# Kernel tuning notes

Hardware: AMD Instinct MI355X
Metric: run time of the kernel (lower is better)

## Reference

```python
import jax, jax.numpy as jnp
import numpy as np

V, D, S, L, H, R, W = 32000, 512, 1536, 4, 4, 32, 128
HFF = int(2.0 * D)
N = S + 1          # anchor node at index 0 + S tokens
K = W + 2          # anchor edge + (W+1) causal window edges
LN_EPS = 1e-5


def _layer_norm(x, g, b):
    m = jnp.mean(x, axis=-1, keepdims=True)
    v = jnp.mean((x - m) ** 2, axis=-1, keepdims=True)
    return (x - m) * jax.lax.rsqrt(v + LN_EPS) * g + b


def _neighbors():
    # windowed causal neighborhood: node i sees nodes i-W..i, plus anchor (node 0)
    pos = jnp.arange(N)
    offs = jnp.arange(-W, 1)                     # W+1 offsets
    idx_w = pos[:, None] + offs[None, :]         # [N, W+1]
    valid_w = idx_w >= 0
    idx_w = jnp.maximum(idx_w, 0)
    anchor_valid = (pos > W)[:, None]            # avoid double-counting anchor when already in window
    idx = jnp.concatenate([jnp.zeros((N, 1), idx_w.dtype), idx_w], axis=1)   # [N, K]
    mask = jnp.concatenate([anchor_valid, valid_w], axis=1)                  # [N, K]
    return idx, mask


def setup_inputs() -> dict:
    key = jax.random.key(0)
    ks = jax.random.split(key, 10)
    std = 0.02
    return {
        'input_ids': jax.random.randint(ks[0], (1, S), 0, V),
        'embed': jax.random.normal(ks[1], (V, D), jnp.float32) * std,
        'pos_emb': jax.random.normal(ks[2], (S, D), jnp.float32) * std,
        'ln_in_g': jnp.ones((D,), jnp.float32),
        'ln_in_b': jnp.zeros((D,), jnp.float32),
        'anchor_state': jnp.zeros((), jnp.float32),
        'anchor_val': jax.random.normal(ks[3], (D,), jnp.float32) * std,
        'state_w': jax.random.normal(ks[4], (D,), jnp.float32) * std,
        'state_b': jnp.zeros((), jnp.float32),
        'wq': jax.random.normal(ks[5], (L, H, D, R), jnp.float32) * std,
        'wk': jax.random.normal(ks[6], (L, H, D, R), jnp.float32) * std,
        'gate': jnp.full((L,), 0.1, jnp.float32),
        'ln_g': jnp.ones((L, D), jnp.float32),
        'ln_b': jnp.zeros((L, D), jnp.float32),
        'ffn_w1': jax.random.normal(ks[7], (L, D, HFF), jnp.float32) * std,
        'ffn_b1': jnp.zeros((L, HFF), jnp.float32),
        'ffn_w2': jax.random.normal(ks[8], (L, HFF, D), jnp.float32) * std,
        'ffn_b2': jnp.zeros((L, D), jnp.float32),
        'ln2_g': jnp.ones((L, D), jnp.float32),
        'ln2_b': jnp.zeros((L, D), jnp.float32),
    }


def reference(input_ids, embed, pos_emb, ln_in_g, ln_in_b, anchor_state, anchor_val,
              state_w, state_b, wq, wk, gate, ln_g, ln_b,
              ffn_w1, ffn_b1, ffn_w2, ffn_b2, ln2_g, ln2_b):
    B = input_ids.shape[0]
    # token embedding + learned position encoding + input norm
    tok = embed[input_ids] + pos_emb[None]                 # [B,S,D]
    tok = _layer_norm(tok, ln_in_g, ln_in_b)
    tok_state = tok @ state_w + state_b                    # [B,S] scalar state per node
    # prepend anchor node
    val = jnp.concatenate([jnp.broadcast_to(anchor_val, (B, 1, D)), tok], axis=1)       # [B,N,D]
    state = jnp.concatenate([jnp.broadcast_to(anchor_state, (B, 1)), tok_state], axis=1)  # [B,N]
    idx, mask = _neighbors()
    scale = 1.0 / np.sqrt(R)
    for l in range(L):
        # low-rank multi-head pairwise scores on windowed neighborhood
        q = jnp.einsum('bnd,hdr->bnhr', val, wq[l])
        k = jnp.einsum('bnd,hdr->bnhr', val, wk[l])
        kg = k[:, idx]                                     # [B,N,K,H,R] gather
        s = jnp.einsum('bnhr,bnkhr->bnkh', q, kg) * scale  # [B,N,K,H]
        # signed_smoothmax head aggregation
        hw = jax.nn.softmax(jnp.abs(s), axis=-1)
        a = jnp.sum(s * hw, axis=-1)                       # [B,N,K]
        # signed_abs_softmax edge compression over neighborhood
        absa = jnp.where(mask[None], jnp.abs(a), -jnp.inf)
        e = jnp.sign(a) * jax.nn.softmax(absa, axis=-1)    # masked entries -> 0 weight
        # state-weighted edges
        sg = state[:, idx]                                 # [B,N,K]
        e = e * sg
        val_g = val[:, idx]                                # [B,N,K,D]
        d_val = jnp.einsum('bnk,bnkd->bnd', e, val_g)
        d_state = jnp.sum(e, axis=-1)
        # gated residual + post-norm
        state = state + gate[l] * d_state
        val = val + gate[l] * d_val
        val = _layer_norm(val, ln_g[l], ln_b[l])
        # value feed-forward (pre-norm, residual scale 1.0)
        h = jax.nn.gelu(_layer_norm(val, ln2_g[l], ln2_b[l]) @ ffn_w1[l] + ffn_b1[l], approximate=False)
        val = val + h @ ffn_w2[l] + ffn_b2[l]
    return val
```

## Files before the change

kernel.cpp:

```cpp
#include <hip/hip_runtime.h>
#include <hip/hip_bf16.h>
#include <stdint.h>

namespace {

constexpr int D    = 512;
constexpr int S    = 1536;
constexpr int N    = S + 1;
constexpr int L    = 4;
constexpr int H    = 4;
constexpr int R    = 32;
constexpr int W    = 128;
constexpr int HFF  = 1024;
constexpr float EPS = 1e-5f;

constexpr int TB   = 4;
constexpr int NB4  = (N + TB - 1) / TB;
constexpr int SP   = 133;
constexpr int SPAD = 137;

constexpr int GS2  = 1024;
constexpr int SLABR = 528;
constexpr int BK   = 128;

typedef __attribute__((ext_vector_type(8))) short short8;
typedef __attribute__((ext_vector_type(4))) float floatx4;

__device__ inline ushort f2bf(float x){
  __hip_bfloat16 h = __float2bfloat16(x);
  return *reinterpret_cast<ushort*>(&h);
}
__device__ inline float bf2f(uint u){
  union { uint u; float f; } c; c.u = u << 16; return c.f;
}

__device__ inline float wave_sum(float v){
#pragma unroll
  for (int o = 32; o; o >>= 1) v += __shfl_xor(v, o, 64);
  return v;
}
__device__ inline float wave_max(float v){
#pragma unroll
  for (int o = 32; o; o >>= 1) v = fmaxf(v, __shfl_xor(v, o, 64));
  return v;
}
__device__ inline float block_sum(float v, float* scr){
  v = wave_sum(v);
  __syncthreads();
  if ((threadIdx.x & 63) == 0) scr[threadIdx.x >> 6] = v;
  __syncthreads();
  return scr[0] + scr[1] + scr[2] + scr[3];
}

__global__ __launch_bounds__(256) void setup_kernel(
    const int* __restrict__ ids, const float* __restrict__ embed,
    const float* __restrict__ pos, const float* __restrict__ g,
    const float* __restrict__ b, const float* __restrict__ anchor_val,
    const float* __restrict__ anchor_state, const float* __restrict__ state_w,
    const float* __restrict__ state_b, float* __restrict__ val,
    ushort* __restrict__ valbf, float* __restrict__ state,
    const float* __restrict__ wq, const float* __restrict__ wk,
    ushort* __restrict__ wqkbf,
    const float* __restrict__ ffn_w1, const float* __restrict__ ffn_w2,
    ushort* __restrict__ w1t, ushort* __restrict__ w2t)
{
  __shared__ float scr[4];
  __shared__ float tile[32 * 33];
  const int t = threadIdx.x;

  for (int n = blockIdx.x; n < N; n += GS2){
    if (n == 0){
      float a0 = anchor_val[t], a1 = anchor_val[t + 256];
      val[t] = a0; val[t + 256] = a1;
      valbf[t] = f2bf(a0); valbf[t + 256] = f2bf(a1);
      if (t == 0) state[0] = anchor_state[0];
      continue;
    }
    int tp = n - 1;
    int id = ids[tp];
    float x0 = embed[(size_t)id * D + t]       + pos[tp * D + t];
    float x1 = embed[(size_t)id * D + t + 256] + pos[tp * D + t + 256];
    float mean = block_sum(x0 + x1, scr) * (1.f / D);
    float var  = block_sum(x0 * x0 + x1 * x1, scr) * (1.f / D) - mean * mean;
    float rs   = rsqrtf(var + EPS);
    float y0 = (x0 - mean) * rs * g[t]       + b[t];
    float y1 = (x1 - mean) * rs * g[t + 256] + b[t + 256];
    val[n * D + t]       = y0;
    val[n * D + t + 256] = y1;
    valbf[n * D + t]       = f2bf(y0);
    valbf[n * D + t + 256] = f2bf(y1);
    float ts = block_sum(y0 * state_w[t] + y1 * state_w[t + 256], scr);
    if (t == 0) state[n] = ts + state_b[0];
  }

  for (int i = blockIdx.x * 256 + t; i < L * 256 * D; i += GS2 * 256){
    int d = i & 511;
    int c = (i >> 9) & 255;
    int l = i >> 17;
    int cc = c & 127;
    int h = cc >> 5, r = cc & 31;
    const float* src = (c < 128) ? wq : wk;
    wqkbf[i] = f2bf(src[((l * H + h) * D + d) * R + r]);
  }
  __syncthreads();

  const int tx = t & 31, ty = t >> 5;
  for (int tl = blockIdx.x; tl < 2 * L * 512; tl += GS2){
    const float* s; ushort* dd; int rows, cols, c0, r0;
    if (tl < 2048){
      int ll = tl >> 9, i = tl & 511;
      rows = D; cols = HFF;
      s  = ffn_w1 + (size_t)ll * D * HFF;
      dd = w1t   + (size_t)ll * D * HFF;
      c0 = (i & 31) << 5; r0 = (i >> 5) << 5;
    } else {
      int tl2 = tl - 2048;
      int ll = tl2 >> 9, i = tl2 & 511;
      rows = HFF; cols = D;
      s  = ffn_w2 + (size_t)ll * D * HFF;
      dd = w2t   + (size_t)ll * D * HFF;
      c0 = (i & 15) << 5; r0 = (i >> 4) << 5;
    }
    __syncthreads();
    for (int rr = ty; rr < 32; rr += 8)
      tile[rr * 33 + tx] = s[(size_t)(r0 + rr) * cols + c0 + tx];
    __syncthreads();
    for (int rr = ty; rr < 32; rr += 8)
      dd[(size_t)(c0 + rr) * rows + r0 + tx] = f2bf(tile[tx * 33 + rr]);
  }
}

template<int ACT>
__global__ __launch_bounds__(256) void gemm64(
    const ushort* __restrict__ A, const ushort* __restrict__ Bt,
    const float* __restrict__ bias, const float* __restrict__ resid,
    float* __restrict__ C, ushort* __restrict__ Cbf,
    int M, int Kd, int Nc)
{
  __shared__ ushort As[16 * SLABR];
  __shared__ ushort Bs[16 * SLABR];
  const int row0 = blockIdx.y * 64;
  const int col0 = blockIdx.x * 64;
  const int t = threadIdx.x;
  const int lane = t & 63, w = t >> 6;
  const int wr = w & 1, wc = w >> 1;
  const int q = lane >> 4, lm = lane & 15;

  const int srow = t >> 3, skb = t & 7;
  int ar0 = min(row0 + srow,      M - 1);
  int ar1 = min(row0 + srow + 32, M - 1);
  const ushort* agA0 = A  + (size_t)ar0 * Kd + skb * 8;
  const ushort* agA1 = A  + (size_t)ar1 * Kd + skb * 8;
  const ushort* agB0 = Bt + (size_t)(col0 + srow) * Kd + skb * 8;
  const ushort* agB1 = Bt + (size_t)(col0 + srow + 32) * Kd + skb * 8;
  ushort* asw00 = &As[ skb      * SLABR +  srow       * 8];
  ushort* asw01 = &As[(skb + 8) * SLABR +  srow       * 8];
  ushort* asw10 = &As[ skb      * SLABR + (srow + 32) * 8];
  ushort* asw11 = &As[(skb + 8) * SLABR + (srow + 32) * 8];
  ushort* bsw00 = &Bs[ skb      * SLABR +  srow       * 8];
  ushort* bsw01 = &Bs[(skb + 8) * SLABR +  srow       * 8];
  ushort* bsw10 = &Bs[ skb      * SLABR + (srow + 32) * 8];
  ushort* bsw11 = &Bs[(skb + 8) * SLABR + (srow + 32) * 8];

  const ushort* arp = &As[(wr * 32 + lm) * 8];
  const ushort* brp = &Bs[(wc * 32 + lm) * 8];

  floatx4 acc[2][2];
#pragma unroll
  for (int m = 0; m < 2; ++m)
#pragma unroll
    for (int n = 0; n < 2; ++n) acc[m][n] = {0.f, 0.f, 0.f, 0.f};

  const int nk0 = Kd / BK;
  uint4 pa0, pa1, pa2, pa3, pb0, pb1, pb2, pb3;
  pa0 = *(const uint4*)(agA0);      pa1 = *(const uint4*)(agA0 + 64);
  pa2 = *(const uint4*)(agA1);      pa3 = *(const uint4*)(agA1 + 64);
  pb0 = *(const uint4*)(agB0);      pb1 = *(const uint4*)(agB0 + 64);
  pb2 = *(const uint4*)(agB1);      pb3 = *(const uint4*)(agB1 + 64);

  for (int i = 0; i < nk0; ++i){
    *(uint4*)asw00 = pa0; *(uint4*)asw01 = pa1;
    *(uint4*)asw10 = pa2; *(uint4*)asw11 = pa3;
    *(uint4*)bsw00 = pb0; *(uint4*)bsw01 = pb1;
    *(uint4*)bsw10 = pb2; *(uint4*)bsw11 = pb3;
    __syncthreads();
    if (i + 1 < nk0){
      const int ko = (i + 1) * BK;
      pa0 = *(const uint4*)(agA0 + ko);      pa1 = *(const uint4*)(agA0 + ko + 64);
      pa2 = *(const uint4*)(agA1 + ko);      pa3 = *(const uint4*)(agA1 + ko + 64);
      pb0 = *(const uint4*)(agB0 + ko);      pb1 = *(const uint4*)(agB0 + ko + 64);
      pb2 = *(const uint4*)(agB1 + ko);      pb3 = *(const uint4*)(agB1 + ko + 64);
    }
#pragma unroll
    for (int kk = 0; kk < 4; ++kk){
      const int kb = (kk * 4 + q) * SLABR;
      short8 am0 = *(const short8*)(arp + kb);
      short8 am1 = *(const short8*)(arp + kb + 16 * 8);
      short8 bn0 = *(const short8*)(brp + kb);
      short8 bn1 = *(const short8*)(brp + kb + 16 * 8);
      acc[0][0] = __builtin_amdgcn_mfma_f32_16x16x32_bf16(am0, bn0, acc[0][0], 0, 0, 0);
      acc[0][1] = __builtin_amdgcn_mfma_f32_16x16x32_bf16(am0, bn1, acc[0][1], 0, 0, 0);
      acc[1][0] = __builtin_amdgcn_mfma_f32_16x16x32_bf16(am1, bn0, acc[1][0], 0, 0, 0);
      acc[1][1] = __builtin_amdgcn_mfma_f32_16x16x32_bf16(am1, bn1, acc[1][1], 0, 0, 0);
    }
    __syncthreads();
  }

#pragma unroll
  for (int m = 0; m < 2; ++m){
#pragma unroll
    for (int n = 0; n < 2; ++n){
      int col = col0 + wc * 32 + n * 16 + lm;
#pragma unroll
      for (int r = 0; r < 4; ++r){
        int row = row0 + wr * 32 + m * 16 + q * 4 + r;
        if (row >= M) continue;
        float v = acc[m][n][r] + (bias ? bias[col] : 0.f);
        if (ACT == 1) v = 0.5f * v * (1.f + erff(v * 0.70710678118654752f));
        if (resid) v += resid[(size_t)row * Nc + col];
        size_t o = (size_t)row * Nc + col;
        if (C)   C[o] = v;
        if (Cbf) Cbf[o] = f2bf(v);
      }
    }
  }
}

__global__ __launch_bounds__(256) void attn4_kernel(
    const ushort* __restrict__ qkbf, const float* __restrict__ val0,
    const ushort* __restrict__ val0bf, const float* __restrict__ state_in,
    float* __restrict__ val1, ushort* __restrict__ x2bf,
    float* __restrict__ state_out,
    const float* __restrict__ gate_p, const float* __restrict__ lng,
    const float* __restrict__ lnb, const float* __restrict__ ln2g,
    const float* __restrict__ ln2b)
{
  __shared__ float kg[64 * SPAD];
  __shared__ float qsh[TB * 128];
  __shared__ float ssh[16 * SPAD];
  __shared__ float ash[TB * SPAD];
  const int n0 = blockIdx.x * TB;
  const int t = threadIdx.x;
  const int w = t >> 6, l = t & 63;
  const float gate = gate_p[0];
  const float scale = 0.17677669529663687f;

#pragma unroll
  for (int i = t; i < TB * 128; i += 256){
    int it = i >> 7, ch = i & 127;
    int gr = min(n0 + it, N - 1);
    qsh[i] = bf2f((uint)qkbf[(size_t)gr * 256 + ch]);
  }

  for (int half = 0; half < 2; ++half){
    for (int i = t; i < SP * 16; i += 256){
      int c = i >> 4, c4 = i & 15;
      int g = (c == 132) ? 0 : min(max(n0 - W + c, 0), N - 1);
      uint2 v = *(const uint2*)&qkbf[(size_t)g * 256 + 128 + half * 64 + c4 * 4];
      int ch = c4 * 4;
      kg[(ch + 0) * SPAD + c] = bf2f(v.x & 0xffffu);
      kg[(ch + 1) * SPAD + c] = bf2f(v.x >> 16);
      kg[(ch + 2) * SPAD + c] = bf2f(v.y & 0xffffu);
      kg[(ch + 3) * SPAD + c] = bf2f(v.y >> 16);
    }
    __syncthreads();
    for (int tk = t; tk < TB * 2 * SP; tk += 256){
      int c = tk % SP;
      int th = tk / SP;
      int tok = th & 3, hh = th >> 2;
      int h = half * 2 + hh;
      const float* qs = &qsh[tok * 128 + h * 32];
      const float* ks = &kg[hh * 32 * SPAD + c];
      float acc = 0.f;
#pragma unroll
      for (int r = 0; r < 32; ++r) acc += qs[r] * ks[r * SPAD];
      ssh[(tok * 4 + h) * SPAD + c] = acc * scale;
    }
    __syncthreads();
  }

  for (int i = t; i < TB * SP; i += 256){
    int tok = i / SP, c = i - tok * SP;
    const float* sr = &ssh[tok * 4 * SPAD + c];
    float s0 = sr[0], s1 = sr[SPAD], s2 = sr[2 * SPAD], s3 = sr[3 * SPAD];
    float a0 = fabsf(s0), a1 = fabsf(s1), a2 = fabsf(s2), a3 = fabsf(s3);
    float m = fmaxf(fmaxf(a0, a1), fmaxf(a2, a3));
    float w0 = expf(a0 - m), w1 = expf(a1 - m), w2 = expf(a2 - m), w3 = expf(a3 - m);
    ash[tok * SPAD + c] = (s0 * w0 + s1 * w1 + s2 * w2 + s3 * w3) / (w0 + w1 + w2 + w3);
  }
  __syncthreads();

  {
    const int n = n0 + w;
    float* arow = &ash[w * SPAD];
    float a0 = arow[l];
    float a1 = arow[64 + l];
    float a2 = (l < 5) ? arow[128 + l] : 0.f;
    bool ok0 = (l >= w) && (n0 - W + l >= 0);
    bool ok1 = (n0 - W + 64 + l >= 0);
    bool ok2;
    if (l < 4)       ok2 = (l <= w);
    else if (l == 4) ok2 = (n > W);
    else             ok2 = false;
    float cand = -3.4e38f;
    if (ok0) cand = fabsf(a0);
    if (ok1) cand = fmaxf(cand, fabsf(a1));
    if (ok2) cand = fmaxf(cand, fabsf(a2));
    float m = wave_max(cand);
    float e0 = ok0 ? expf(fabsf(a0) - m) : 0.f;
    float e1 = ok1 ? expf(fabsf(a1) - m) : 0.f;
    float e2 = ok2 ? expf(fabsf(a2) - m) : 0.f;
    float inv = 1.f / wave_sum(e0 + e1 + e2);
    int g0 = min(max(n0 - W + l, 0), N - 1);
    int g1 = min(max(n0 - W + 64 + l, 0), N - 1);
    int g2 = (l < 4) ? min(n0 + l, N - 1) : 0;
    float sg0 = (a0 > 0.f) ? 1.f : ((a0 < 0.f) ? -1.f : 0.f);
    float sg1 = (a1 > 0.f) ? 1.f : ((a1 < 0.f) ? -1.f : 0.f);
    float sg2 = (a2 > 0.f) ? 1.f : ((a2 < 0.f) ? -1.f : 0.f);
    float t0 = sg0 * e0 * inv * state_in[g0];
    float t1 = sg1 * e1 * inv * state_in[g1];
    float t2 = (l < 5) ? sg2 * e2 * inv * state_in[g2] : 0.f;
    arow[l] = t0;
    arow[64 + l] = t1;
    if (l < 5) arow[128 + l] = t2;
    float ds = wave_sum(t0 + t1 + t2);
    if (l == 0 && n < N) state_out[n] = state_in[n] + gate * ds;
  }
  __syncthreads();

  float acc[TB][2];
#pragma unroll
  for (int k = 0; k < TB; ++k){ acc[k][0] = 0.f; acc[k][1] = 0.f; }
  {
    const int d0 = 2 * t;
    for (int c = 0; c < SP; ++c){
      int g = (c == 132) ? 0 : min(max(n0 - W + c, 0), N - 1);
      uint v = *(const uint*)&val0bf[(size_t)g * D + d0];
      float vx = bf2f(v & 0xffffu), vy = bf2f(v >> 16);
#pragma unroll
      for (int k = 0; k < TB; ++k){
        float e = ash[k * SPAD + c];
        acc[k][0] += e * vx;
        acc[k][1] += e * vy;
      }
    }
  }
  float* xbuf = kg;
  {
    const int d0 = 2 * t;
#pragma unroll
    for (int k = 0; k < TB; ++k){
      int nc = min(n0 + k, N - 1);
      float2 vv = *(const float2*)&val0[(size_t)nc * D + d0];
      xbuf[k * 520 + d0]     = vv.x + gate * acc[k][0];
      xbuf[k * 520 + d0 + 1] = vv.y + gate * acc[k][1];
    }
  }
  __syncthreads();

  {
    const int n = n0 + w;
    const int d = l * 8;
    const float* xr = &xbuf[w * 520 + d];
    float x[8];
#pragma unroll
    for (int j = 0; j < 8; ++j) x[j] = xr[j];
    float s1 = 0.f, s2 = 0.f;
#pragma unroll
    for (int j = 0; j < 8; ++j){ s1 += x[j]; s2 += x[j] * x[j]; }
    s1 = wave_sum(s1); s2 = wave_sum(s2);
    float mean = s1 * (1.f / D);
    float var  = s2 * (1.f / D) - mean * mean;
    float rs   = rsqrtf(var + EPS);
    float y[8];
    float u1 = 0.f, u2 = 0.f;
#pragma unroll
    for (int j = 0; j < 8; ++j){
      float yv = (x[j] - mean) * rs * lng[d + j] + lnb[d + j];
      y[j] = yv; u1 += yv; u2 += yv * yv;
    }
    u1 = wave_sum(u1); u2 = wave_sum(u2);
    float mean2 = u1 * (1.f / D);
    float var2  = u2 * (1.f / D) - mean2 * mean2;
    float rs2   = rsqrtf(var2 + EPS);
    if (n < N){
      *(float4*)&val1[(size_t)n * D + d]     = make_float4(y[0], y[1], y[2], y[3]);
      *(float4*)&val1[(size_t)n * D + d + 4] = make_float4(y[4], y[5], y[6], y[7]);
      uint4 pk;
      uint z0 = f2bf((y[0] - mean2) * rs2 * ln2g[d + 0] + ln2b[d + 0]);
      uint z1 = f2bf((y[1] - mean2) * rs2 * ln2g[d + 1] + ln2b[d + 1]);
      uint z2 = f2bf((y[2] - mean2) * rs2 * ln2g[d + 2] + ln2b[d + 2]);
      uint z3 = f2bf((y[3] - mean2) * rs2 * ln2g[d + 3] + ln2b[d + 3]);
      uint z4 = f2bf((y[4] - mean2) * rs2 * ln2g[d + 4] + ln2b[d + 4]);
      uint z5 = f2bf((y[5] - mean2) * rs2 * ln2g[d + 5] + ln2b[d + 5]);
      uint z6 = f2bf((y[6] - mean2) * rs2 * ln2g[d + 6] + ln2b[d + 6]);
      uint z7 = f2bf((y[7] - mean2) * rs2 * ln2g[d + 7] + ln2b[d + 7]);
      pk.x = z0 | (z1 << 16); pk.y = z2 | (z3 << 16);
      pk.z = z4 | (z5 << 16); pk.w = z6 | (z7 << 16);
      *(uint4*)&x2bf[(size_t)n * D + d] = pk;
    }
  }
}

}

extern "C" void kernel_launch(void* const* d_in, const int* in_sizes, int n_in,
                              void* d_out, int out_size, void* d_ws, size_t ws_size,
                              hipStream_t stream)
{
  (void)in_sizes; (void)n_in; (void)out_size; (void)ws_size;
  const int*   ids          = (const int*)d_in[0];
  const float* embed        = (const float*)d_in[1];
  const float* pos_emb      = (const float*)d_in[2];
  const float* ln_in_g      = (const float*)d_in[3];
  const float* ln_in_b      = (const float*)d_in[4];
  const float* anchor_state = (const float*)d_in[5];
  const float* anchor_val   = (const float*)d_in[6];
  const float* state_w      = (const float*)d_in[7];
  const float* state_b      = (const float*)d_in[8];
  const float* wq           = (const float*)d_in[9];
  const float* wk           = (const float*)d_in[10];
  const float* gate         = (const float*)d_in[11];
  const float* ln_g         = (const float*)d_in[12];
  const float* ln_b         = (const float*)d_in[13];
  const float* ffn_w1       = (const float*)d_in[14];
  const float* ffn_b1       = (const float*)d_in[15];
  const float* ffn_w2       = (const float*)d_in[16];
  const float* ffn_b2       = (const float*)d_in[17];
  const float* ln2_g        = (const float*)d_in[18];
  const float* ln2_b        = (const float*)d_in[19];
  float* out = (float*)d_out;

  float* wsf  = (float*)d_ws;
  float* val0 = wsf;  wsf += (size_t)N * D;
  float* val1 = wsf;  wsf += (size_t)N * D;
  ushort* wsu   = (ushort*)wsf;
  ushort* val0bf = wsu;  wsu += (size_t)N * D;
  ushort* x2bf   = wsu;  wsu += (size_t)N * D;
  ushort* hbf    = wsu;  wsu += (size_t)N * HFF;
  ushort* qkbf   = wsu;  wsu += (size_t)N * 256;
  ushort* wqkbf  = wsu;  wsu += (size_t)L * 256 * D;
  ushort* w1t    = wsu;  wsu += (size_t)L * HFF * D;
  ushort* w2t    = wsu;  wsu += (size_t)L * HFF * D;
  float* st0 = (float*)wsu;
  float* st1 = st0 + N;

  setup_kernel<<<GS2, 256, 0, stream>>>(
      ids, embed, pos_emb, ln_in_g, ln_in_b, anchor_val, anchor_state,
      state_w, state_b, val0, val0bf, st0,
      wq, wk, wqkbf, ffn_w1, ffn_w2, w1t, w2t);

  float* sin_  = st0;
  float* sout_ = st1;
  const int MT64 = (N + 63) / 64;
  for (int l = 0; l < L; ++l){
    gemm64<0><<<dim3(256 / 64, MT64), 256, 0, stream>>>(
        val0bf, wqkbf + (size_t)l * 256 * D, nullptr, nullptr,
        nullptr, qkbf, N, D, 256);
    attn4_kernel<<<NB4, 256, 0, stream>>>(qkbf, val0, val0bf, sin_, val1, x2bf,
                                          sout_, gate + l, ln_g + l * D,
                                          ln_b + l * D, ln2_g + l * D,
                                          ln2_b + l * D);
    gemm64<1><<<dim3(HFF / 64, MT64), 256, 0, stream>>>(
        x2bf, w1t + (size_t)l * HFF * D, ffn_b1 + l * HFF, nullptr,
        nullptr, hbf, N, D, HFF);
    float* dst = (l == L - 1) ? out : val0;
    gemm64<0><<<dim3(D / 64, MT64), 256, 0, stream>>>(
        hbf, w2t + (size_t)l * HFF * D, ffn_b2 + l * D, val1,
        dst, val0bf, N, HFF, D);
    float* tmp = sin_; sin_ = sout_; sout_ = tmp;
  }
}
```

Before: 374.9 us.

## Fuse Q/K projection into attention kernel, recomputing window keys per block

Removes the separate Q/K projection GEMM and its bf16 round trip through global memory. Each attention block now computes its own 4 query rows and the keys for its 133-row window with bf16 MFMA, staging val0bf and the projection weights in shared memory. This saves one launch and the intermediate buffer. In exchange, each block recomputes keys for a window that overlaps heavily with its neighbours, so total projection work grows many-fold. Each block also re-reads the full projection weight slice.

```diff
diff --git a/kernel.cpp b/kernel.cpp
--- a/kernel.cpp
+++ b/kernel.cpp
@@ -22,6 +22,10 @@
 constexpr int GS2  = 1024;
 constexpr int SLABR = 528;
 constexpr int BK   = 128;
+
+constexpr int KROWS = 144;
+constexpr int SLABK = KROWS * 8 + 8;
+constexpr int BSLAB = 64 * 8 + 8;
 
 typedef __attribute__((ext_vector_type(8))) short short8;
 typedef __attribute__((ext_vector_type(4))) float floatx4;
@@ -226,8 +230,9 @@
   }
 }
 
-__global__ __launch_bounds__(256) void attn4_kernel(
-    const ushort* __restrict__ qkbf, const float* __restrict__ val0,
+__global__ __launch_bounds__(256) void qkattn_kernel(
+    const ushort* __restrict__ wqk,
+    const float* __restrict__ val0,
     const ushort* __restrict__ val0bf, const float* __restrict__ state_in,
     float* __restrict__ val1, ushort* __restrict__ x2bf,
     float* __restrict__ state_out,
@@ -239,29 +244,99 @@
   __shared__ float qsh[TB * 128];
   __shared__ float ssh[16 * SPAD];
   __shared__ float ash[TB * SPAD];
+  __shared__ ushort As2[8 * SLABK];
+  __shared__ ushort Bs2[8 * BSLAB];
   const int n0 = blockIdx.x * TB;
   const int t = threadIdx.x;
   const int w = t >> 6, l = t & 63;
+  const int q = l >> 4, lm = l & 15;
   const float gate = gate_p[0];
   const float scale = 0.17677669529663687f;
 
-#pragma unroll
-  for (int i = t; i < TB * 128; i += 256){
-    int it = i >> 7, ch = i & 127;
-    int gr = min(n0 + it, N - 1);
-    qsh[i] = bf2f((uint)qkbf[(size_t)gr * 256 + ch]);
-  }
+  {
+    floatx4 accq0 = {0.f,0.f,0.f,0.f}, accq1 = {0.f,0.f,0.f,0.f};
+    for (int ks = 0; ks < 8; ++ks){
+      if (t < 128){
+        int row = t >> 3, kb = t & 7;
+        int g = min(n0 + row, N - 1);
+        *(uint4*)&Bs2[kb * BSLAB + row * 8] =
+            *(const uint4*)&val0bf[(size_t)g * D + ks * 64 + kb * 8];
+      }
+#pragma unroll
+      for (int s = 0; s < 4; ++s){
+        int slot = t + s * 256;
+        int ch = slot >> 3, kb = slot & 7;
+        *(uint4*)&As2[kb * SLABK + ch * 8] =
+            *(const uint4*)&wqk[(size_t)ch * D + ks * 64 + kb * 8];
+      }
+      __syncthreads();
+#pragma unroll
+      for (int kk = 0; kk < 2; ++kk){
+        int kc = kk * 4 + q;
+        short8 a  = *(const short8*)&Bs2[kc * BSLAB + lm * 8];
+        short8 b0 = *(const short8*)&As2[kc * SLABK + ((2 * w)     * 16 + lm) * 8];
+        short8 b1 = *(const short8*)&As2[kc * SLABK + ((2 * w + 1) * 16 + lm) * 8];
+        accq0 = __builtin_amdgcn_mfma_f32_16x16x32_bf16(a, b0, accq0, 0, 0, 0);
+        accq1 = __builtin_amdgcn_mfma_f32_16x16x32_bf16(a, b1, accq1, 0, 0, 0);
+      }
+      __syncthreads();
+    }
+    if (q == 0){
+#pragma unroll
+      for (int r = 0; r < 4; ++r){
+        qsh[r * 128 + (2 * w)     * 16 + lm] = accq0[r];
+        qsh[r * 128 + (2 * w + 1) * 16 + lm] = accq1[r];
+      }
+    }
+  }
+  __syncthreads();
 
   for (int half = 0; half < 2; ++half){
-    for (int i = t; i < SP * 16; i += 256){
-      int c = i >> 4, c4 = i & 15;
-      int g = (c == 132) ? 0 : min(max(n0 - W + c, 0), N - 1);
-      uint2 v = *(const uint2*)&qkbf[(size_t)g * 256 + 128 + half * 64 + c4 * 4];
-      int ch = c4 * 4;
-      kg[(ch + 0) * SPAD + c] = bf2f(v.x & 0xffffu);
-      kg[(ch + 1) * SPAD + c] = bf2f(v.x >> 16);
-      kg[(ch + 2) * SPAD + c] = bf2f(v.y & 0xffffu);
-      kg[(ch + 3) * SPAD + c] = bf2f(v.y >> 16);
+    floatx4 acck[9];
+#pragma unroll
+    for (int tr = 0; tr < 9; ++tr) acck[tr] = {0.f, 0.f, 0.f, 0.f};
+    for (int ks = 0; ks < 8; ++ks){
+#pragma unroll
+      for (int s = 0; s < 5; ++s){
+        int slot = t + s * 256;
+        if (slot < KROWS * 8){
+          int row = slot >> 3, kb = slot & 7;
+          int g = (row == 132) ? 0 : min(max(n0 - W + row, 0), N - 1);
+          *(uint4*)&As2[kb * SLABK + row * 8] =
+              *(const uint4*)&val0bf[(size_t)g * D + ks * 64 + kb * 8];
+        }
+      }
+#pragma unroll
+      for (int s = 0; s < 2; ++s){
+        int slot = t + s * 256;
+        int ch = slot >> 3, kb = slot & 7;
+        *(uint4*)&Bs2[kb * BSLAB + ch * 8] =
+            *(const uint4*)&wqk[(size_t)(128 + half * 64 + ch) * D + ks * 64 + kb * 8];
+      }
+      __syncthreads();
+#pragma unroll
+      for (int kk = 0; kk < 2; ++kk){
+        int kc = kk * 4 + q;
+        short8 b = *(const short8*)&Bs2[kc * BSLAB + (w * 16 + lm) * 8];
+#pragma unroll
+        for (int tr = 0; tr < 9; ++tr){
+          short8 a = *(const short8*)&As2[kc * SLABK + (tr * 16 + lm) * 8];
+          acck[tr] = __builtin_amdgcn_mfma_f32_16x16x32_bf16(a, b, acck[tr], 0, 0, 0);
+        }
+      }
+      __syncthreads();
+    }
+    {
+      int ch = w * 16 + lm;
+#pragma unroll
+      for (int tr = 0; tr < 9; ++tr){
+        int cbase = tr * 16 + q * 4;
+#pragma unroll
+        for (int r = 0; r < 4; ++r){
+          int c = cbase + r;
+          if (c <= 132) kg[ch * SPAD + c] = acck[tr][r];
+        }
+      }
     }
     __syncthreads();
     for (int tk = t; tk < TB * 2 * SP; tk += 256){
@@ -270,10 +345,10 @@
       int tok = th & 3, hh = th >> 2;
       int h = half * 2 + hh;
       const float* qs = &qsh[tok * 128 + h * 32];
-      const float* ks = &kg[hh * 32 * SPAD + c];
+      const float* ks2 = &kg[hh * 32 * SPAD + c];
       float acc = 0.f;
 #pragma unroll
-      for (int r = 0; r < 32; ++r) acc += qs[r] * ks[r * SPAD];
+      for (int r = 0; r < 32; ++r) acc += qs[r] * ks2[r * SPAD];
       ssh[(tok * 4 + h) * SPAD + c] = acc * scale;
     }
     __syncthreads();
@@ -438,7 +513,6 @@
   ushort* val0bf = wsu;  wsu += (size_t)N * D;
   ushort* x2bf   = wsu;  wsu += (size_t)N * D;
   ushort* hbf    = wsu;  wsu += (size_t)N * HFF;
-  ushort* qkbf   = wsu;  wsu += (size_t)N * 256;
   ushort* wqkbf  = wsu;  wsu += (size_t)L * 256 * D;
   ushort* w1t    = wsu;  wsu += (size_t)L * HFF * D;
   ushort* w2t    = wsu;  wsu += (size_t)L * HFF * D;
@@ -454,13 +528,10 @@
   float* sout_ = st1;
   const int MT64 = (N + 63) / 64;
   for (int l = 0; l < L; ++l){
-    gemm64<0><<<dim3(256 / 64, MT64), 256, 0, stream>>>(
-        val0bf, wqkbf + (size_t)l * 256 * D, nullptr, nullptr,
-        nullptr, qkbf, N, D, 256);
-    attn4_kernel<<<NB4, 256, 0, stream>>>(qkbf, val0, val0bf, sin_, val1, x2bf,
-                                          sout_, gate + l, ln_g + l * D,
-                                          ln_b + l * D, ln2_g + l * D,
-                                          ln2_b + l * D);
+    qkattn_kernel<<<NB4, 256, 0, stream>>>(
+        wqkbf + (size_t)l * 256 * D, val0, val0bf, sin_, val1, x2bf,
+        sout_, gate + l, ln_g + l * D, ln_b + l * D, ln2_g + l * D,
+        ln2_b + l * D);
     gemm64<1><<<dim3(HFF / 64, MT64), 256, 0, stream>>>(
         x2bf, w1t + (size_t)l * HFF * D, ffn_b1 + l * HFF, nullptr,
         nullptr, hbf, N, D, HFF);
```

After: 453.2 us. +20.9%, slower.

## Fuse attention, FFN and next-layer QK projection into one per-layer kernel

Applied to the files above, without the earlier changes.

Replaces the per-layer sequence of QK GEMM, attention, FFN1 and FFN2 kernels with a single mega-kernel. Each 4-token block runs attention, then both FFN matmuls with MFMA, then the next layer's QK projection, keeping all intermediates in LDS. Ping-pong buffers hold the values and qk, and only the first layer's QK GEMM is launched separately. This removes the global round-trips for x2, h and val1 and cuts launch count. The cost is that every block streams the full layer weights from global or L2, and the 16-row MFMA tiles carry only 4 useful rows.

```diff
diff --git a/kernel.cpp b/kernel.cpp
--- a/kernel.cpp
+++ b/kernel.cpp
@@ -22,6 +22,8 @@
 constexpr int GS2  = 1024;
 constexpr int SLABR = 528;
 constexpr int BK   = 128;
+
+constexpr int SMB = 48080;
 
 typedef __attribute__((ext_vector_type(8))) short short8;
 typedef __attribute__((ext_vector_type(4))) float floatx4;
@@ -226,22 +228,39 @@
   }
 }
 
-__global__ __launch_bounds__(256) void attn4_kernel(
-    const ushort* __restrict__ qkbf, const float* __restrict__ val0,
-    const ushort* __restrict__ val0bf, const float* __restrict__ state_in,
-    float* __restrict__ val1, ushort* __restrict__ x2bf,
+__global__ __launch_bounds__(256) void mega_kernel(
+    const ushort* __restrict__ qkc,
+    const ushort* __restrict__ wqkn,
+    const float* __restrict__ val0,
+    const ushort* __restrict__ val0bf,
+    const float* __restrict__ state_in,
+    float* __restrict__ dstf,
+    ushort* __restrict__ v0bfn,
+    ushort* __restrict__ qkn,
     float* __restrict__ state_out,
     const float* __restrict__ gate_p, const float* __restrict__ lng,
     const float* __restrict__ lnb, const float* __restrict__ ln2g,
-    const float* __restrict__ ln2b)
+    const float* __restrict__ ln2b,
+    const float* __restrict__ b1p, const float* __restrict__ b2p,
+    const ushort* __restrict__ w1l, const ushort* __restrict__ w2l,
+    int last)
 {
-  __shared__ float kg[64 * SPAD];
-  __shared__ float qsh[TB * 128];
-  __shared__ float ssh[16 * SPAD];
-  __shared__ float ash[TB * SPAD];
+  __shared__ __align__(16) char SM[SMB];
+  float* SMf = (float*)SM;
+  float* kg  = SMf;
+  float* qsh = SMf + 8768;
+  float* ssh = SMf + 9280;
+  float* ash = SMf + 11472;
+  float* val1s = SMf + 8768;
+  ushort* x2u = (ushort*)(SM + 8320);
+  ushort* hsu = (ushort*)(SM + 12544);
+  ushort* v0u = (ushort*)(SM + 20864);
+
   const int n0 = blockIdx.x * TB;
   const int t = threadIdx.x;
   const int w = t >> 6, l = t & 63;
+  const int q = l >> 4, lm = l & 15;
+  const int arow = lm & 3;
   const float gate = gate_p[0];
   const float scale = 0.17677669529663687f;
 
@@ -249,14 +268,14 @@
   for (int i = t; i < TB * 128; i += 256){
     int it = i >> 7, ch = i & 127;
     int gr = min(n0 + it, N - 1);
-    qsh[i] = bf2f((uint)qkbf[(size_t)gr * 256 + ch]);
+    qsh[i] = bf2f((uint)qkc[(size_t)gr * 256 + ch]);
   }
 
   for (int half = 0; half < 2; ++half){
     for (int i = t; i < SP * 16; i += 256){
       int c = i >> 4, c4 = i & 15;
       int g = (c == 132) ? 0 : min(max(n0 - W + c, 0), N - 1);
-      uint2 v = *(const uint2*)&qkbf[(size_t)g * 256 + 128 + half * 64 + c4 * 4];
+      uint2 v = *(const uint2*)&qkc[(size_t)g * 256 + 128 + half * 64 + c4 * 4];
       int ch = c4 * 4;
       kg[(ch + 0) * SPAD + c] = bf2f(v.x & 0xffffu);
       kg[(ch + 1) * SPAD + c] = bf2f(v.x >> 16);
@@ -292,10 +311,10 @@
 
   {
     const int n = n0 + w;
-    float* arow = &ash[w * SPAD];
-    float a0 = arow[l];
-    float a1 = arow[64 + l];
-    float a2 = (l < 5) ? arow[128 + l] : 0.f;
+    float* arw = &ash[w * SPAD];
+    float a0 = arw[l];
+    float a1 = arw[64 + l];
+    float a2 = (l < 5) ? arw[128 + l] : 0.f;
     bool ok0 = (l >= w) && (n0 - W + l >= 0);
     bool ok1 = (n0 - W + 64 + l >= 0);
     bool ok2;
@@ -320,9 +339,9 @@
     float t0 = sg0 * e0 * inv * state_in[g0];
     float t1 = sg1 * e1 * inv * state_in[g1];
     float t2 = (l < 5) ? sg2 * e2 * inv * state_in[g2] : 0.f;
-    arow[l] = t0;
-    arow[64 + l] = t1;
-    if (l < 5) arow[128 + l] = t2;
+    arw[l] = t0;
+    arw[64 + l] = t1;
+    if (l < 5) arw[128 + l] = t2;
     float ds = wave_sum(t0 + t1 + t2);
     if (l == 0 && n < N) state_out[n] = state_in[n] + gate * ds;
   }
@@ -359,7 +378,6 @@
   __syncthreads();
 
   {
-    const int n = n0 + w;
     const int d = l * 8;
     const float* xr = &xbuf[w * 520 + d];
     float x[8];
@@ -383,21 +401,108 @@
     float mean2 = u1 * (1.f / D);
     float var2  = u2 * (1.f / D) - mean2 * mean2;
     float rs2   = rsqrtf(var2 + EPS);
-    if (n < N){
-      *(float4*)&val1[(size_t)n * D + d]     = make_float4(y[0], y[1], y[2], y[3]);
-      *(float4*)&val1[(size_t)n * D + d + 4] = make_float4(y[4], y[5], y[6], y[7]);
-      uint4 pk;
-      uint z0 = f2bf((y[0] - mean2) * rs2 * ln2g[d + 0] + ln2b[d + 0]);
-      uint z1 = f2bf((y[1] - mean2) * rs2 * ln2g[d + 1] + ln2b[d + 1]);
-      uint z2 = f2bf((y[2] - mean2) * rs2 * ln2g[d + 2] + ln2b[d + 2]);
-      uint z3 = f2bf((y[3] - mean2) * rs2 * ln2g[d + 3] + ln2b[d + 3]);
-      uint z4 = f2bf((y[4] - mean2) * rs2 * ln2g[d + 4] + ln2b[d + 4]);
-      uint z5 = f2bf((y[5] - mean2) * rs2 * ln2g[d + 5] + ln2b[d + 5]);
-      uint z6 = f2bf((y[6] - mean2) * rs2 * ln2g[d + 6] + ln2b[d + 6]);
-      uint z7 = f2bf((y[7] - mean2) * rs2 * ln2g[d + 7] + ln2b[d + 7]);
-      pk.x = z0 | (z1 << 16); pk.y = z2 | (z3 << 16);
-      pk.z = z4 | (z5 << 16); pk.w = z6 | (z7 << 16);
-      *(uint4*)&x2bf[(size_t)n * D + d] = pk;
+    *(float4*)&val1s[w * 520 + d]     = make_float4(y[0], y[1], y[2], y[3]);
+    *(float4*)&val1s[w * 520 + d + 4] = make_float4(y[4], y[5], y[6], y[7]);
+    uint4 pk;
+    uint z0 = f2bf((y[0] - mean2) * rs2 * ln2g[d + 0] + ln2b[d + 0]);
+    uint z1 = f2bf((y[1] - mean2) * rs2 * ln2g[d + 1] + ln2b[d + 1]);
+    uint z2 = f2bf((y[2] - mean2) * rs2 * ln2g[d + 2] + ln2b[d + 2]);
+    uint z3 = f2bf((y[3] - mean2) * rs2 * ln2g[d + 3] + ln2b[d + 3]);
+    uint z4 = f2bf((y[4] - mean2) * rs2 * ln2g[d + 4] + ln2b[d + 4]);
+    uint z5 = f2bf((y[5] - mean2) * rs2 * ln2g[d + 5] + ln2b[d + 5]);
+    uint z6 = f2bf((y[6] - mean2) * rs2 * ln2g[d + 6] + ln2b[d + 6]);
+    uint z7 = f2bf((y[7] - mean2) * rs2 * ln2g[d + 7] + ln2b[d + 7]);
+    pk.x = z0 | (z1 << 16); pk.y = z2 | (z3 << 16);
+    pk.z = z4 | (z5 << 16); pk.w = z6 | (z7 << 16);
+    *(uint4*)&x2u[w * 528 + d] = pk;
+  }
+  __syncthreads();
+
+  for (int ct = 0; ct < 8; ++ct){
+    int c0 = w * 256 + ct * 32;
+    int c1 = c0 + 16;
+    floatx4 f0 = {0.f,0.f,0.f,0.f}, f1 = {0.f,0.f,0.f,0.f};
+#pragma unroll
+    for (int s = 0; s < 16; ++s){
+      short8 av = *(const short8*)&x2u[arow * 528 + s * 32 + q * 8];
+      short8 b0 = *(const short8*)&w1l[(size_t)(c0 + lm) * 512 + s * 32 + q * 8];
+      short8 b1 = *(const short8*)&w1l[(size_t)(c1 + lm) * 512 + s * 32 + q * 8];
+      f0 = __builtin_amdgcn_mfma_f32_16x16x32_bf16(av, b0, f0, 0, 0, 0);
+      f1 = __builtin_amdgcn_mfma_f32_16x16x32_bf16(av, b1, f1, 0, 0, 0);
+    }
+    if (q == 0){
+#pragma unroll
+      for (int r = 0; r < 4; ++r){
+        float v0 = f0[r] + b1p[c0 + lm];
+        float v1 = f1[r] + b1p[c1 + lm];
+        v0 = 0.5f * v0 * (1.f + erff(v0 * 0.70710678118654752f));
+        v1 = 0.5f * v1 * (1.f + erff(v1 * 0.70710678118654752f));
+        hsu[r * 1040 + c0 + lm] = f2bf(v0);
+        hsu[r * 1040 + c1 + lm] = f2bf(v1);
+      }
+    }
+  }
+  __syncthreads();
+
+  for (int ct = 0; ct < 4; ++ct){
+    int c0 = w * 128 + ct * 32;
+    int c1 = c0 + 16;
+    floatx4 f0 = {0.f,0.f,0.f,0.f}, f1 = {0.f,0.f,0.f,0.f};
+#pragma unroll
+    for (int s = 0; s < 32; ++s){
+      short8 av = *(const short8*)&hsu[arow * 1040 + s * 32 + q * 8];
+      short8 b0 = *(const short8*)&w2l[(size_t)(c0 + lm) * 1024 + s * 32 + q * 8];
+      short8 b1 = *(const short8*)&w2l[(size_t)(c1 + lm) * 1024 + s * 32 + q * 8];
+      f0 = __builtin_amdgcn_mfma_f32_16x16x32_bf16(av, b0, f0, 0, 0, 0);
+      f1 = __builtin_amdgcn_mfma_f32_16x16x32_bf16(av, b1, f1, 0, 0, 0);
+    }
+    if (q == 0){
+#pragma unroll
+      for (int r = 0; r < 4; ++r){
+        int n = n0 + r;
+        float v0 = f0[r] + b2p[c0 + lm] + val1s[r * 520 + c0 + lm];
+        float v1 = f1[r] + b2p[c1 + lm] + val1s[r * 520 + c1 + lm];
+        ushort h0 = f2bf(v0), h1 = f2bf(v1);
+        if (n < N){
+          dstf[(size_t)n * D + c0 + lm] = v0;
+          dstf[(size_t)n * D + c1 + lm] = v1;
+          if (!last){
+            v0bfn[(size_t)n * D + c0 + lm] = h0;
+            v0bfn[(size_t)n * D + c1 + lm] = h1;
+          }
+        }
+        if (!last){
+          v0u[r * 528 + c0 + lm] = h0;
+          v0u[r * 528 + c1 + lm] = h1;
+        }
+      }
+    }
+  }
+
+  if (!last){
+    __syncthreads();
+    for (int ct = 0; ct < 2; ++ct){
+      int c0 = w * 64 + ct * 32;
+      int c1 = c0 + 16;
+      floatx4 f0 = {0.f,0.f,0.f,0.f}, f1 = {0.f,0.f,0.f,0.f};
+#pragma unroll
+      for (int s = 0; s < 16; ++s){
+        short8 av = *(const short8*)&v0u[arow * 528 + s * 32 + q * 8];
+        short8 b0 = *(const short8*)&wqkn[(size_t)(c0 + lm) * 512 + s * 32 + q * 8];
+        short8 b1 = *(const short8*)&wqkn[(size_t)(c1 + lm) * 512 + s * 32 + q * 8];
+        f0 = __builtin_amdgcn_mfma_f32_16x16x32_bf16(av, b0, f0, 0, 0, 0);
+        f1 = __builtin_amdgcn_mfma_f32_16x16x32_bf16(av, b1, f1, 0, 0, 0);
+      }
+      if (q == 0){
+#pragma unroll
+        for (int r = 0; r < 4; ++r){
+          int n = n0 + r;
+          if (n < N){
+            qkn[(size_t)n * 256 + c0 + lm] = f2bf(f0[r]);
+            qkn[(size_t)n * 256 + c1 + lm] = f2bf(f1[r]);
+          }
+        }
+      }
     }
   }
 }
@@ -432,42 +537,46 @@
   float* out = (float*)d_out;
 
   float* wsf  = (float*)d_ws;
-  float* val0 = wsf;  wsf += (size_t)N * D;
-  float* val1 = wsf;  wsf += (size_t)N * D;
-  ushort* wsu   = (ushort*)wsf;
-  ushort* val0bf = wsu;  wsu += (size_t)N * D;
-  ushort* x2bf   = wsu;  wsu += (size_t)N * D;
-  ushort* hbf    = wsu;  wsu += (size_t)N * HFF;
-  ushort* qkbf   = wsu;  wsu += (size_t)N * 256;
-  ushort* wqkbf  = wsu;  wsu += (size_t)L * 256 * D;
-  ushort* w1t    = wsu;  wsu += (size_t)L * HFF * D;
-  ushort* w2t    = wsu;  wsu += (size_t)L * HFF * D;
+  float* val0a = wsf;  wsf += (size_t)N * D;
+  float* val0b = wsf;  wsf += (size_t)N * D;
+  ushort* wsu    = (ushort*)wsf;
+  ushort* val0bfa = wsu;  wsu += (size_t)N * D;
+  ushort* val0bfb = wsu;  wsu += (size_t)N * D;
+  ushort* qka     = wsu;  wsu += (size_t)N * 256;
+  ushort* qkb     = wsu;  wsu += (size_t)N * 256;
+  ushort* wqkbf   = wsu;  wsu += (size_t)L * 256 * D;
+  ushort* w1t     = wsu;  wsu += (size_t)L * HFF * D;
+  ushort* w2t     = wsu;  wsu += (size_t)L * HFF * D;
   float* st0 = (float*)wsu;
   float* st1 = st0 + N;
 
   setup_kernel<<<GS2, 256, 0, stream>>>(
       ids, embed, pos_emb, ln_in_g, ln_in_b, anchor_val, anchor_state,
-      state_w, state_b, val0, val0bf, st0,
+      state_w, state_b, val0a, val0bfa, st0,
       wq, wk, wqkbf, ffn_w1, ffn_w2, w1t, w2t);
 
-  float* sin_  = st0;
-  float* sout_ = st1;
   const int MT64 = (N + 63) / 64;
+  gemm64<0><<<dim3(256 / 64, MT64), 256, 0, stream>>>(
+      val0bfa, wqkbf, nullptr, nullptr, nullptr, qka, N, D, 256);
+
+  float*  v0c  = val0a;  float*  v0n  = val0b;
+  ushort* v0bc = val0bfa; ushort* v0bn = val0bfb;
+  ushort* qkc  = qka;    ushort* qkn  = qkb;
+  float*  sin_ = st0;    float*  sout_ = st1;
+
   for (int l = 0; l < L; ++l){
-    gemm64<0><<<dim3(256 / 64, MT64), 256, 0, stream>>>(
-        val0bf, wqkbf + (size_t)l * 256 * D, nullptr, nullptr,
-        nullptr, qkbf, N, D, 256);
-    attn4_kernel<<<NB4, 256, 0, stream>>>(qkbf, val0, val0bf, sin_, val1, x2bf,
-                                          sout_, gate + l, ln_g + l * D,
-                                          ln_b + l * D, ln2_g + l * D,
-                                          ln2_b + l * D);
-    gemm64<1><<<dim3(HFF / 64, MT64), 256, 0, stream>>>(
-        x2bf, w1t + (size_t)l * HFF * D, ffn_b1 + l * HFF, nullptr,
-        nullptr, hbf, N, D, HFF);
-    float* dst = (l == L - 1) ? out : val0;
-    gemm64<0><<<dim3(D / 64, MT64), 256, 0, stream>>>(
-        hbf, w2t + (size_t)l * HFF * D, ffn_b2 + l * D, val1,
-        dst, val0bf, N, HFF, D);
-    float* tmp = sin_; sin_ = sout_; sout_ = tmp;
-  }
-}
+    int last = (l == L - 1);
+    mega_kernel<<<NB4, 256, 0, stream>>>(
+        qkc, last ? nullptr : (wqkbf + (size_t)(l + 1) * 256 * D),
+        v0c, v0bc, sin_,
+        last ? out : v0n, last ? nullptr : v0bn, last ? nullptr : qkn,
+        sout_,
+        gate + l, ln_g + l * D, ln_b + l * D, ln2_g + l * D, ln2_b + l * D,
+        ffn_b1 + l * HFF, ffn_b2 + l * D,
+        w1t + (size_t)l * HFF * D, w2t + (size_t)l * HFF * D, last);
+    float*  tf = v0c;  v0c  = v0n;  v0n  = tf;
+    ushort* tu = v0bc; v0bc = v0bn; v0bn = tu;
+    tu = qkc; qkc = qkn; qkn = tu;
+    float* ts = sin_; sin_ = sout_; sout_ = ts;
+  }
+}
```

Measured after the change: 735.9 us. +96.3%, slower.
